# Optimization experiments

Hardware: AMD Instinct MI355X
Metric: run time of the kernel (lower is better)

Reference implementation:

```python
import jax, jax.numpy as jnp
import numpy as np

B, S, D = 2, 2048, 2048
H, DN, DR, DV, R = 16, 128, 64, 128, 512
EPS = 1e-6


def rmsnorm(x, g, eps=EPS):
    var = jnp.mean(x * x, axis=-1, keepdims=True)
    return x * jax.lax.rsqrt(var + eps) * g


def apply_rope(x, freqs):
    # x: [B,S,H,DR], freqs: [S, DR//2] angles. Complex-pair (interleaved) rotation.
    b, s, h, d = x.shape
    xp = x.reshape(b, s, h, d // 2, 2)
    xr, xi = xp[..., 0], xp[..., 1]
    cos = jnp.cos(freqs)[None, :, None, :]
    sin = jnp.sin(freqs)[None, :, None, :]
    outr = xr * cos - xi * sin
    outi = xr * sin + xi * cos
    return jnp.stack([outr, outi], axis=-1).reshape(b, s, h, d)


def setup_inputs() -> dict:
    key = jax.random.key(0)
    ks = jax.random.split(key, 8)
    x = jax.random.normal(ks[0], (B, S, D), dtype=jnp.float32)
    # RoPE angles: pos * inv_freq, standard theta=10000
    inv_freq = 1.0 / (10000.0 ** (np.arange(0, DR, 2, dtype=np.float32) / DR))
    freqs = jnp.asarray(np.arange(S, dtype=np.float32)[:, None] * inv_freq[None, :])
    sc = lambda fan_in: 1.0 / np.sqrt(fan_in)
    # weights stored [in, out] so forward is x @ W
    w_kv = jax.random.normal(ks[1], (D, R), dtype=jnp.float32) * sc(D)
    g_kv = jnp.ones((R,), dtype=jnp.float32)
    w_k = jax.random.normal(ks[2], (R, H * (DN + DR)), dtype=jnp.float32) * sc(R)
    w_v = jax.random.normal(ks[3], (R, H * DV), dtype=jnp.float32) * sc(R)
    w_qn = jax.random.normal(ks[4], (D, H * DN), dtype=jnp.float32) * sc(D)
    w_qr = jax.random.normal(ks[5], (D, H * DR), dtype=jnp.float32) * sc(D)
    w_o = jax.random.normal(ks[6], (H * DV, D), dtype=jnp.float32) * sc(H * DV)
    return {"x": x, "freqs": freqs, "w_kv": w_kv, "g_kv": g_kv, "w_k": w_k,
            "w_v": w_v, "w_qn": w_qn, "w_qr": w_qr, "w_o": w_o}


def reference(x, freqs, w_kv, g_kv, w_k, w_v, w_qn, w_qr, w_o):
    b, s, _ = x.shape
    # latent KV compression + RMSNorm
    kv = rmsnorm(x @ w_kv, g_kv)                       # [B,S,R]
    k_full = (kv @ w_k).reshape(b, s, H, DN + DR)      # [B,S,H,192]
    k_nope, k_rope = k_full[..., :DN], k_full[..., DN:]
    v = (kv @ w_v).reshape(b, s, H, DV)                # [B,S,H,DV]
    q_nope = (x @ w_qn).reshape(b, s, H, DN)
    q_rope = (x @ w_qr).reshape(b, s, H, DR)
    q_rope = apply_rope(q_rope, freqs)
    k_rope = apply_rope(k_rope, freqs)
    q = jnp.concatenate([q_nope, q_rope], axis=-1)     # [B,S,H,192]
    k = jnp.concatenate([k_nope, k_rope], axis=-1)
    scale = 1.0 / np.sqrt(DN + DR)
    scores = jnp.einsum('bshd,bthd->bhst', q, k) * scale  # [B,H,S,S]
    causal = jnp.tril(jnp.ones((s, s), dtype=bool))
    scores = jnp.where(causal[None, None], scores, jnp.float32(-1e30))
    attn = jax.nn.softmax(scores, axis=-1)
    out = jnp.einsum('bhst,bthd->bshd', attn, v).reshape(b, s, H * DV)
    return out @ w_o                                   # [B,S,D]
```

## Files before the change

### kernel.cpp

```cpp
#include <hip/hip_runtime.h>

typedef __bf16 bf16_t;
typedef bf16_t bf16x8 __attribute__((ext_vector_type(8)));
typedef bf16_t bf16x4v __attribute__((ext_vector_type(4)));
typedef float f32x4 __attribute__((ext_vector_type(4)));

#define GLDS16(g, l) __builtin_amdgcn_global_load_lds( \
    (const __attribute__((address_space(1))) void*)(g), \
    (__attribute__((address_space(3))) void*)(l), 16, 0, 0)

#define BB 2
#define SEQ 2048
#define DMODEL 2048
#define RDIM 512
#define NH 16
#define DNOPE 128
#define DROPE 64
#define DVDIM 128
#define MROWS 4096
#define DQK 192


__global__ __launch_bounds__(256) void cast_x_kernel(const float* __restrict__ x,
                                                     bf16_t* __restrict__ xb) {
    int idx = blockIdx.x * 256 + threadIdx.x;
    float4 v = ((const float4*)x)[idx];
    bf16x4v o;
    o[0] = (bf16_t)v.x; o[1] = (bf16_t)v.y; o[2] = (bf16_t)v.z; o[3] = (bf16_t)v.w;
    ((bf16x4v*)xb)[idx] = o;
}

__global__ __launch_bounds__(256) void wtrans_kernel(const float* __restrict__ W,
                                                     bf16_t* __restrict__ WT,
                                                     int K, int N) {
    __shared__ float t[32][33];
    int n0 = blockIdx.x * 32, k0 = blockIdx.y * 32;
    int tx = threadIdx.x & 31, ty = threadIdx.x >> 5;
    #pragma unroll
    for (int i = 0; i < 4; ++i)
        t[ty + i*8][tx] = W[(size_t)(k0 + ty + i*8) * N + n0 + tx];
    __syncthreads();
    #pragma unroll
    for (int i = 0; i < 4; ++i)
        WT[(size_t)(n0 + ty + i*8) * K + k0 + tx] = (bf16_t)t[tx][ty + i*8];
}

__global__ __launch_bounds__(256) void rope_table_kernel(const float* __restrict__ freqs,
                                                         float* __restrict__ costab,
                                                         float* __restrict__ sintab) {
    int idx = blockIdx.x * 256 + threadIdx.x;
    float f = freqs[idx];
    costab[idx] = cosf(f);
    sintab[idx] = sinf(f);
}

__global__ __launch_bounds__(256) void rmsnorm_kernel(const float* __restrict__ kvf,
                                                      const float* __restrict__ gkv,
                                                      bf16_t* __restrict__ kvb) {
    int m = blockIdx.x;
    int tid = threadIdx.x;
    const float* rowp = kvf + (size_t)m * RDIM;
    float2 v = *(const float2*)(rowp + tid * 2);
    float ss = v.x * v.x + v.y * v.y;
    #pragma unroll
    for (int d = 1; d < 64; d <<= 1) ss += __shfl_xor(ss, d, 64);
    __shared__ float red[4];
    if ((tid & 63) == 0) red[tid >> 6] = ss;
    __syncthreads();
    float tot = red[0] + red[1] + red[2] + red[3];
    float scale = rsqrtf(tot * (1.0f / RDIM) + 1e-6f);
    bf16_t* orow = kvb + (size_t)m * RDIM;
    orow[tid*2]     = (bf16_t)(v.x * scale * gkv[tid*2]);
    orow[tid*2 + 1] = (bf16_t)(v.y * scale * gkv[tid*2 + 1]);
}


template<typename OutT, int EPI>
__global__ __launch_bounds__(256, 2) void gemm_bt(const bf16_t* __restrict__ A,
                                                  const bf16_t* __restrict__ Bt,
                                                  OutT* __restrict__ C,
                                                  int M, int N, int K,
                                                  const float* __restrict__ costab,
                                                  const float* __restrict__ sintab) {
    __shared__ __align__(16) char ldsA[128 * 128];
    __shared__ __align__(16) char ldsB[128 * 128];
    int tid = threadIdx.x;
    int lane = tid & 63, wave = tid >> 6;
    int n0 = blockIdx.x * 128, m0 = blockIdx.y * 128;
    int wr = wave >> 1, wc = wave & 1;
    int g = lane >> 4, c = lane & 15;
    f32x4 acc[4][4] = {};

    int srow = tid >> 3;
    int sch = tid & 7;

    int nkt = K >> 6;
    for (int kt = 0; kt < nkt; ++kt) {
        int k0 = kt << 6;
        #pragma unroll
        for (int j = 0; j < 4; ++j) {
            int row = j * 32 + srow;
            int csrc = sch ^ (row & 7);
            const char* gA = (const char*)(A + (size_t)(m0 + row) * K + k0) + csrc * 16;
            const char* gB = (const char*)(Bt + (size_t)(n0 + row) * K + k0) + csrc * 16;
            char* lA = ldsA + j * 4096 + wave * 1024;
            char* lB = ldsB + j * 4096 + wave * 1024;
            GLDS16(gA, lA);
            GLDS16(gB, lB);
        }
        __syncthreads();
        #pragma unroll
        for (int kk = 0; kk < 2; ++kk) {
            int kb = kk * 64 + g * 16;
            bf16x8 aF[4], bF[4];
            #pragma unroll
            for (int m = 0; m < 4; ++m) {
                int row = wr * 64 + m * 16 + c;
                aF[m] = *(const bf16x8*)(ldsA + row * 128 + (kb ^ ((row & 7) << 4)));
            }
            #pragma unroll
            for (int n = 0; n < 4; ++n) {
                int row = wc * 64 + n * 16 + c;
                bF[n] = *(const bf16x8*)(ldsB + row * 128 + (kb ^ ((row & 7) << 4)));
            }
            #pragma unroll
            for (int m = 0; m < 4; ++m)
                #pragma unroll
                for (int n = 0; n < 4; ++n)
                    acc[m][n] = __builtin_amdgcn_mfma_f32_16x16x32_bf16(aF[m], bF[n], acc[m][n], 0, 0, 0);
        }
        __syncthreads();
    }
    #pragma unroll
    for (int m = 0; m < 4; ++m) {
        int grow0 = m0 + wr * 64 + m * 16 + g * 4;
        #pragma unroll
        for (int n = 0; n < 4; ++n) {
            int gcol = n0 + wc * 64 + n * 16 + c;
            bool rope = false;
            int j = 0;
            if (EPI == 1) {
                rope = (gcol < 3072) && ((gcol % 192) >= 128);
                j = ((gcol % 192) - 128) >> 1;
            } else if (EPI == 2) {
                rope = (gcol >= 2048);
                j = ((gcol - 2048) & 63) >> 1;
            }
            if (EPI != 0 && rope) {
                bool even = (c & 1) == 0;
                #pragma unroll
                for (int i = 0; i < 4; ++i) {
                    float v = acc[m][n][i];
                    float pv = __shfl_xor(v, 1, 64);
                    int s = (grow0 + i) & (SEQ - 1);
                    float cs = costab[s * 32 + j], sn = sintab[s * 32 + j];
                    float o = even ? (v * cs - pv * sn) : (pv * sn + v * cs);
                    C[(size_t)(grow0 + i) * N + gcol] = (OutT)o;
                }
            } else {
                #pragma unroll
                for (int i = 0; i < 4; ++i)
                    C[(size_t)(grow0 + i) * N + gcol] = (OutT)acc[m][n][i];
            }
        }
    }
}

__global__ __launch_bounds__(256) void pack_v_kernel(const bf16_t* __restrict__ kvout,
                                                     bf16_t* __restrict__ vt) {
    __shared__ bf16_t t[64][144];
    int blk = blockIdx.x;
    int bh = blk >> 5, st = blk & 31;
    int s0 = st * 64;
    int b = bh >> 4, h = bh & 15;
    int tid = threadIdx.x;
    #pragma unroll
    for (int i = 0; i < 4; ++i) {
        int id = i * 256 + tid;
        int row = id >> 4, ch = id & 15;
        bf16x8 v = *(const bf16x8*)(kvout + (size_t)(b * SEQ + s0 + row) * 5120 + 3072 + h * 128 + ch * 8);
        *(bf16x8*)&t[row][ch * 8] = v;
    }
    __syncthreads();
    #pragma unroll
    for (int i = 0; i < 4; ++i) {
        int id = i * 256 + tid;
        int dv = id >> 3, sc = id & 7;
        bf16x8 v;
        #pragma unroll
        for (int jj = 0; jj < 8; ++jj) v[jj] = t[sc * 8 + jj][dv];
        *(bf16x8*)(vt + ((size_t)bh * 128 + dv) * SEQ + s0 + sc * 8) = v;
    }
}


__global__ __launch_bounds__(512, 2) void attn_kernel(const bf16_t* __restrict__ Qf,
                                                      const bf16_t* __restrict__ KV,
                                                      const bf16_t* __restrict__ VT,
                                                      bf16_t* __restrict__ O) {
    __shared__ __align__(16) char ldsK[2 * 64 * 384];
    __shared__ __align__(16) char ldsV[2 * 128 * 128];
    __shared__ __align__(16) char ldsP[8 * 16 * 176];
    int tid = threadIdx.x, lane = tid & 63, wave = tid >> 6;
    int g = lane >> 4, c = lane & 15;

    int bid = blockIdx.x;
    int xcd = bid & 7, r = bid >> 3;
    int bh = xcd * 4 + (r & 3);
    int p = r >> 2;
    int b = bh >> 4, h = bh & 15;

    const bf16_t* Kb = KV + (size_t)b * SEQ * 5120 + h * DQK;
    const bf16_t* Vb = VT + (size_t)bh * 128 * SEQ;
    char* ldsPw = ldsP + wave * (16 * 176);

    size_t soff[3];
    #pragma unroll
    for (int i2 = 0; i2 < 3; ++i2) {
        int id = i2 * 512 + tid;
        int row = id / 24, ch = id - row * 24;
        soff[i2] = (size_t)row * 10240 + (ch ^ (row & 7)) * 16;
    }
    size_t voff[2];
    #pragma unroll
    for (int i2 = 0; i2 < 2; ++i2) {
        int id = i2 * 512 + tid;
        int row = id >> 3, ch = id & 7;
        voff[i2] = (size_t)row * (SEQ * 2) + (ch ^ (row & 7)) * 16;
    }
    const float sc = 0.0721687836f * 1.44269504f;

    bf16x8 vones;
    #pragma unroll
    for (int j = 0; j < 8; ++j) vones[j] = (bf16_t)1.0f;

    #pragma unroll 1
    for (int pass = 0; pass < 2; ++pass) {
        int qt = pass ? p : (15 - p);
        int q0 = qt * 128;
        int nt = 2 * qt + 2;
        int tdiag = 2 * qt + (wave >> 2);

        bf16x8 qf[6];
        {
            int qrow = q0 + wave * 16 + c;
            const bf16_t* qn = Qf + (size_t)(b * SEQ + qrow) * 3072 + h * DNOPE + g * 8;
            #pragma unroll
            for (int kk = 0; kk < 4; ++kk) qf[kk] = *(const bf16x8*)(qn + kk * 32);
            const bf16_t* qr = Qf + (size_t)(b * SEQ + qrow) * 3072 + 2048 + h * DROPE + g * 8;
            qf[4] = *(const bf16x8*)(qr);
            qf[5] = *(const bf16x8*)(qr + 32);
        }
        float m_run[4];
        f32x4 accO[9] = {};
        #pragma unroll
        for (int i = 0; i < 4; ++i) m_run[i] = -3.0e38f;

        {
            const char* Kt = (const char*)(Kb);
            #pragma unroll
            for (int i2 = 0; i2 < 3; ++i2)
                GLDS16(Kt + soff[i2], ldsK + i2 * 8192 + wave * 1024);
            const char* Vt = (const char*)Vb;
            #pragma unroll
            for (int i2 = 0; i2 < 2; ++i2)
                GLDS16(Vt + voff[i2], ldsV + i2 * 8192 + wave * 1024);
        }
        __syncthreads();

        #pragma unroll 1
        for (int t = 0; t < nt; ++t) {
            int cur = t & 1;
            if (t + 1 < nt) {
                int nxt = cur ^ 1;
                const char* Kt = (const char*)(Kb + (size_t)(t + 1) * 64 * 5120);
                #pragma unroll
                for (int i2 = 0; i2 < 3; ++i2)
                    GLDS16(Kt + soff[i2], ldsK + nxt * 24576 + i2 * 8192 + wave * 1024);
                const char* Vt = (const char*)Vb + (size_t)(t + 1) * 128;
                #pragma unroll
                for (int i2 = 0; i2 < 2; ++i2)
                    GLDS16(Vt + voff[i2], ldsV + nxt * 16384 + i2 * 8192 + wave * 1024);
            }

            if (t <= tdiag) {
                bool diag = (t == tdiag);
                const char* ldsKc = ldsK + cur * 24576;
                const char* ldsVc = ldsV + cur * 16384;

                f32x4 accS[4] = {};
                __builtin_amdgcn_s_setprio(1);
                #pragma unroll
                for (int kk = 0; kk < 6; ++kk) {
                    int kb = kk * 64 + g * 16;
                    #pragma unroll
                    for (int n = 0; n < 4; ++n) {
                        int row = n * 16 + c;
                        bf16x8 kf = *(const bf16x8*)(ldsKc + row * 384 + (kb ^ ((row & 7) << 4)));
                        accS[n] = __builtin_amdgcn_mfma_f32_16x16x32_bf16(qf[kk], kf, accS[n], 0, 0, 0);
                    }
                }
                __builtin_amdgcn_s_setprio(0);

                #pragma unroll
                for (int n = 0; n < 4; ++n)
                    #pragma unroll
                    for (int i = 0; i < 4; ++i) {
                        float v = accS[n][i] * sc;
                        if (diag && (n * 16 + c > (wave & 3) * 16 + g * 4 + i)) v = -1e30f;
                        accS[n][i] = v;
                    }
                float mx[4];
                #pragma unroll
                for (int i = 0; i < 4; ++i) {
                    float m2 = fmaxf(fmaxf(accS[0][i], accS[1][i]), fmaxf(accS[2][i], accS[3][i]));
                    #pragma unroll
                    for (int d = 1; d < 16; d <<= 1) m2 = fmaxf(m2, __shfl_xor(m2, d, 64));
                    mx[i] = m2;
                }
                bool nore = __all((mx[0] <= m_run[0] + 8.f) & (mx[1] <= m_run[1] + 8.f) &
                                  (mx[2] <= m_run[2] + 8.f) & (mx[3] <= m_run[3] + 8.f));
                if (nore) {
                    #pragma unroll
                    for (int i = 0; i < 4; ++i)
                        #pragma unroll
                        for (int n = 0; n < 4; ++n)
                            accS[n][i] = exp2f(accS[n][i] - m_run[i]);
                } else {
                    #pragma unroll
                    for (int i = 0; i < 4; ++i) {
                        float mnew = fmaxf(m_run[i], mx[i]);
                        float alpha = exp2f(m_run[i] - mnew);
                        m_run[i] = mnew;
                        #pragma unroll
                        for (int n = 0; n < 4; ++n)
                            accS[n][i] = exp2f(accS[n][i] - mnew);
                        #pragma unroll
                        for (int n = 0; n < 9; ++n) accO[n][i] *= alpha;
                    }
                }
                #pragma unroll
                for (int n = 0; n < 4; ++n)
                    #pragma unroll
                    for (int i = 0; i < 4; ++i)
                        *(bf16_t*)(ldsPw + (g * 4 + i) * 176 + (n * 16 + c) * 2) = (bf16_t)accS[n][i];
                bf16x8 pf0 = *(const bf16x8*)(ldsPw + c * 176 + g * 16);
                bf16x8 pf1 = *(const bf16x8*)(ldsPw + c * 176 + 64 + g * 16);

                __builtin_amdgcn_s_setprio(1);
                #pragma unroll
                for (int n = 0; n < 8; ++n) {
                    int row = n * 16 + c;
                    bf16x8 vf0 = *(const bf16x8*)(ldsVc + row * 128 + ((g * 16) ^ ((c & 7) << 4)));
                    bf16x8 vf1 = *(const bf16x8*)(ldsVc + row * 128 + ((64 + g * 16) ^ ((c & 7) << 4)));
                    accO[n] = __builtin_amdgcn_mfma_f32_16x16x32_bf16(pf0, vf0, accO[n], 0, 0, 0);
                    accO[n] = __builtin_amdgcn_mfma_f32_16x16x32_bf16(pf1, vf1, accO[n], 0, 0, 0);
                }
                accO[8] = __builtin_amdgcn_mfma_f32_16x16x32_bf16(pf0, vones, accO[8], 0, 0, 0);
                accO[8] = __builtin_amdgcn_mfma_f32_16x16x32_bf16(pf1, vones, accO[8], 0, 0, 0);
                __builtin_amdgcn_s_setprio(0);
            }
            __syncthreads();
        }
        float inv_l[4];
        #pragma unroll
        for (int i = 0; i < 4; ++i) inv_l[i] = 1.0f / accO[8][i];
        #pragma unroll
        for (int n = 0; n < 8; ++n) {
            int gcol = h * 128 + n * 16 + c;
            #pragma unroll
            for (int i = 0; i < 4; ++i) {
                int mrow = b * SEQ + q0 + wave * 16 + g * 4 + i;
                O[(size_t)mrow * 2048 + gcol] = (bf16_t)(accO[n][i] * inv_l[i]);
            }
        }
        __syncthreads();
    }
}


extern "C" void kernel_launch(void* const* d_in, const int* in_sizes, int n_in,
                              void* d_out, int out_size, void* d_ws, size_t ws_size,
                              hipStream_t stream) {
    const float* x     = (const float*)d_in[0];
    const float* freqs = (const float*)d_in[1];
    const float* w_kv  = (const float*)d_in[2];
    const float* g_kv  = (const float*)d_in[3];
    const float* w_k   = (const float*)d_in[4];
    const float* w_v   = (const float*)d_in[5];
    const float* w_qn  = (const float*)d_in[6];
    const float* w_qr  = (const float*)d_in[7];
    const float* w_o   = (const float*)d_in[8];
    float* out = (float*)d_out;

    char* ws = (char*)d_ws;
    size_t off = 0;
    auto alloc = [&](size_t bytes) { char* p = ws + off; off += (bytes + 255) & ~(size_t)255; return p; };
    bf16_t* xb     = (bf16_t*)alloc((size_t)MROWS * DMODEL * 2);
    bf16_t* wkvT   = (bf16_t*)alloc((size_t)RDIM * DMODEL * 2);
    bf16_t* wkvwT  = (bf16_t*)alloc((size_t)5120 * RDIM * 2);
    bf16_t* wqT    = (bf16_t*)alloc((size_t)3072 * DMODEL * 2);
    bf16_t* woT    = (bf16_t*)alloc((size_t)DMODEL * DMODEL * 2);
    float*  kvf    = (float*) alloc((size_t)MROWS * RDIM * 4);
    bf16_t* kvb    = (bf16_t*)alloc((size_t)MROWS * RDIM * 2);
    bf16_t* kvout  = (bf16_t*)alloc((size_t)MROWS * 5120 * 2);
    bf16_t* qfull  = (bf16_t*)alloc((size_t)MROWS * 3072 * 2);
    bf16_t* vt     = (bf16_t*)alloc((size_t)32 * 128 * SEQ * 2);
    bf16_t* attno  = (bf16_t*)alloc((size_t)MROWS * 2048 * 2);
    float*  costab = (float*) alloc((size_t)SEQ * 32 * 4);
    float*  sintab = (float*) alloc((size_t)SEQ * 32 * 4);

    cast_x_kernel<<<(MROWS * DMODEL / 4) / 256, 256, 0, stream>>>(x, xb);
    wtrans_kernel<<<dim3(RDIM / 32, DMODEL / 32), 256, 0, stream>>>(w_kv, wkvT, DMODEL, RDIM);
    wtrans_kernel<<<dim3(3072 / 32, RDIM / 32), 256, 0, stream>>>(w_k, wkvwT, RDIM, 3072);
    wtrans_kernel<<<dim3(2048 / 32, RDIM / 32), 256, 0, stream>>>(w_v, wkvwT + (size_t)3072 * RDIM, RDIM, 2048);
    wtrans_kernel<<<dim3(2048 / 32, DMODEL / 32), 256, 0, stream>>>(w_qn, wqT, DMODEL, 2048);
    wtrans_kernel<<<dim3(1024 / 32, DMODEL / 32), 256, 0, stream>>>(w_qr, wqT + (size_t)2048 * DMODEL, DMODEL, 1024);
    wtrans_kernel<<<dim3(2048 / 32, DMODEL / 32), 256, 0, stream>>>(w_o, woT, DMODEL, 2048);
    rope_table_kernel<<<(SEQ * 32) / 256, 256, 0, stream>>>(freqs, costab, sintab);

    gemm_bt<float, 0><<<dim3(RDIM / 128, MROWS / 128), 256, 0, stream>>>(xb, wkvT, kvf, MROWS, RDIM, DMODEL, nullptr, nullptr);
    rmsnorm_kernel<<<MROWS, 256, 0, stream>>>(kvf, g_kv, kvb);
    gemm_bt<bf16_t, 1><<<dim3(5120 / 128, MROWS / 128), 256, 0, stream>>>(kvb, wkvwT, kvout, MROWS, 5120, RDIM, costab, sintab);
    gemm_bt<bf16_t, 2><<<dim3(3072 / 128, MROWS / 128), 256, 0, stream>>>(xb, wqT, qfull, MROWS, 3072, DMODEL, costab, sintab);

    pack_v_kernel<<<32 * 32, 256, 0, stream>>>(kvout, vt);

    attn_kernel<<<256, 512, 0, stream>>>(qfull, kvout, vt, attno);

    gemm_bt<float, 0><<<dim3(2048 / 128, MROWS / 128), 256, 0, stream>>>(attno, woT, out, MROWS, 2048, DMODEL, nullptr, nullptr);
}
```

Measured before the change: 324.2 us.

## Fuse KV-down and Q projections into one GEMM; triple-buffer attention K/V loads

Concatenates w_kv, w_qn and w_qr into one transposed weight so a single GEMM over x produces both the latent KV (fp32) and rope'd Q (bf16) through a new split epilogue. This removes a second full pass over x and a launch, and avoids the under-filled 512-column GEMM grid. The attention kernel moves from double to triple buffering of K/V tiles, using explicit vmcnt waits and one barrier per iteration in place of a trailing __syncthreads. It also pre-scales Q by the softmax scale so the per-element scale multiply is dropped. The extra LDS lowers the headroom for occupancy, and rounding Q after scaling slightly changes numerics.

After: 304.4 us. 6.1% less time.

```diff
diff --git a/kernel.cpp b/kernel.cpp
--- a/kernel.cpp
+++ b/kernel.cpp
@@ -81,7 +81,8 @@
                                                   OutT* __restrict__ C,
                                                   int M, int N, int K,
                                                   const float* __restrict__ costab,
-                                                  const float* __restrict__ sintab) {
+                                                  const float* __restrict__ sintab,
+                                                  bf16_t* __restrict__ C2) {
     __shared__ __align__(16) char ldsA[128 * 128];
     __shared__ __align__(16) char ldsB[128 * 128];
     int tid = threadIdx.x;
@@ -137,30 +138,57 @@
         #pragma unroll
         for (int n = 0; n < 4; ++n) {
             int gcol = n0 + wc * 64 + n * 16 + c;
-            bool rope = false;
-            int j = 0;
-            if (EPI == 1) {
-                rope = (gcol < 3072) && ((gcol % 192) >= 128);
-                j = ((gcol % 192) - 128) >> 1;
-            } else if (EPI == 2) {
-                rope = (gcol >= 2048);
-                j = ((gcol - 2048) & 63) >> 1;
-            }
-            if (EPI != 0 && rope) {
-                bool even = (c & 1) == 0;
-                #pragma unroll
-                for (int i = 0; i < 4; ++i) {
-                    float v = acc[m][n][i];
-                    float pv = __shfl_xor(v, 1, 64);
-                    int s = (grow0 + i) & (SEQ - 1);
-                    float cs = costab[s * 32 + j], sn = sintab[s * 32 + j];
-                    float o = even ? (v * cs - pv * sn) : (pv * sn + v * cs);
-                    C[(size_t)(grow0 + i) * N + gcol] = (OutT)o;
+            if (EPI == 3) {
+                if (gcol < 512) {
+                    #pragma unroll
+                    for (int i = 0; i < 4; ++i)
+                        C[(size_t)(grow0 + i) * 512 + gcol] = (OutT)acc[m][n][i];
+                } else {
+                    int qcol = gcol - 512;
+                    if (qcol >= 2048) {
+                        int j = ((qcol - 2048) & 63) >> 1;
+                        bool even = (c & 1) == 0;
+                        #pragma unroll
+                        for (int i = 0; i < 4; ++i) {
+                            float v = acc[m][n][i];
+                            float pv = __shfl_xor(v, 1, 64);
+                            int s = (grow0 + i) & (SEQ - 1);
+                            float cs = costab[s * 32 + j], sn = sintab[s * 32 + j];
+                            float o = even ? (v * cs - pv * sn) : (pv * sn + v * cs);
+                            C2[(size_t)(grow0 + i) * 3072 + qcol] = (bf16_t)o;
+                        }
+                    } else {
+                        #pragma unroll
+                        for (int i = 0; i < 4; ++i)
+                            C2[(size_t)(grow0 + i) * 3072 + qcol] = (bf16_t)acc[m][n][i];
+                    }
                 }
             } else {
-                #pragma unroll
-                for (int i = 0; i < 4; ++i)
-                    C[(size_t)(grow0 + i) * N + gcol] = (OutT)acc[m][n][i];
+                bool rope = false;
+                int j = 0;
+                if (EPI == 1) {
+                    rope = (gcol < 3072) && ((gcol % 192) >= 128);
+                    j = ((gcol % 192) - 128) >> 1;
+                } else if (EPI == 2) {
+                    rope = (gcol >= 2048);
+                    j = ((gcol - 2048) & 63) >> 1;
+                }
+                if (EPI != 0 && rope) {
+                    bool even = (c & 1) == 0;
+                    #pragma unroll
+                    for (int i = 0; i < 4; ++i) {
+                        float v = acc[m][n][i];
+                        float pv = __shfl_xor(v, 1, 64);
+                        int s = (grow0 + i) & (SEQ - 1);
+                        float cs = costab[s * 32 + j], sn = sintab[s * 32 + j];
+                        float o = even ? (v * cs - pv * sn) : (pv * sn + v * cs);
+                        C[(size_t)(grow0 + i) * N + gcol] = (OutT)o;
+                    }
+                } else {
+                    #pragma unroll
+                    for (int i = 0; i < 4; ++i)
+                        C[(size_t)(grow0 + i) * N + gcol] = (OutT)acc[m][n][i];
+                }
             }
         }
     }
@@ -198,8 +226,8 @@
                                                       const bf16_t* __restrict__ KV,
                                                       const bf16_t* __restrict__ VT,
                                                       bf16_t* __restrict__ O) {
-    __shared__ __align__(16) char ldsK[2 * 64 * 384];
-    __shared__ __align__(16) char ldsV[2 * 128 * 128];
+    __shared__ __align__(16) char ldsK[3 * 64 * 384];
+    __shared__ __align__(16) char ldsV[3 * 128 * 128];
     __shared__ __align__(16) char ldsP[8 * 16 * 176];
     int tid = threadIdx.x, lane = tid & 63, wave = tid >> 6;
     int g = lane >> 4, c = lane & 15;
@@ -233,6 +261,17 @@
     bf16x8 vones;
     #pragma unroll
     for (int j = 0; j < 8; ++j) vones[j] = (bf16_t)1.0f;
+
+    auto stage = [&](int t, int buf) {
+        const char* Kt = (const char*)(Kb + (size_t)t * 64 * 5120);
+        #pragma unroll
+        for (int i2 = 0; i2 < 3; ++i2)
+            GLDS16(Kt + soff[i2], ldsK + buf * 24576 + i2 * 8192 + wave * 1024);
+        const char* Vt = (const char*)Vb + (size_t)t * 128;
+        #pragma unroll
+        for (int i2 = 0; i2 < 2; ++i2)
+            GLDS16(Vt + voff[i2], ldsV + buf * 16384 + i2 * 8192 + wave * 1024);
+    };
 
     #pragma unroll 1
     for (int pass = 0; pass < 2; ++pass) {
@@ -250,38 +289,29 @@
             const bf16_t* qr = Qf + (size_t)(b * SEQ + qrow) * 3072 + 2048 + h * DROPE + g * 8;
             qf[4] = *(const bf16x8*)(qr);
             qf[5] = *(const bf16x8*)(qr + 32);
+            #pragma unroll
+            for (int kk = 0; kk < 6; ++kk)
+                #pragma unroll
+                for (int j = 0; j < 8; ++j)
+                    qf[kk][j] = (bf16_t)((float)qf[kk][j] * sc);
         }
         float m_run[4];
         f32x4 accO[9] = {};
         #pragma unroll
         for (int i = 0; i < 4; ++i) m_run[i] = -3.0e38f;
 
-        {
-            const char* Kt = (const char*)(Kb);
-            #pragma unroll
-            for (int i2 = 0; i2 < 3; ++i2)
-                GLDS16(Kt + soff[i2], ldsK + i2 * 8192 + wave * 1024);
-            const char* Vt = (const char*)Vb;
-            #pragma unroll
-            for (int i2 = 0; i2 < 2; ++i2)
-                GLDS16(Vt + voff[i2], ldsV + i2 * 8192 + wave * 1024);
-        }
-        __syncthreads();
+        stage(0, 0);
+        stage(1, 1);
 
         #pragma unroll 1
         for (int t = 0; t < nt; ++t) {
-            int cur = t & 1;
-            if (t + 1 < nt) {
-                int nxt = cur ^ 1;
-                const char* Kt = (const char*)(Kb + (size_t)(t + 1) * 64 * 5120);
-                #pragma unroll
-                for (int i2 = 0; i2 < 3; ++i2)
-                    GLDS16(Kt + soff[i2], ldsK + nxt * 24576 + i2 * 8192 + wave * 1024);
-                const char* Vt = (const char*)Vb + (size_t)(t + 1) * 128;
-                #pragma unroll
-                for (int i2 = 0; i2 < 2; ++i2)
-                    GLDS16(Vt + voff[i2], ldsV + nxt * 16384 + i2 * 8192 + wave * 1024);
-            }
+            int cur = t - (t / 3) * 3;
+            if (t + 1 < nt) asm volatile("s_waitcnt vmcnt(5)" ::: "memory");
+            else            asm volatile("s_waitcnt vmcnt(0)" ::: "memory");
+            __builtin_amdgcn_s_barrier();
+            __builtin_amdgcn_sched_barrier(0);
+            asm volatile("" ::: "memory");
+            if (t + 2 < nt) stage(t + 2, (t + 2) % 3);
 
             if (t <= tdiag) {
                 bool diag = (t == tdiag);
@@ -302,14 +332,13 @@
                 }
                 __builtin_amdgcn_s_setprio(0);
 
-                #pragma unroll
-                for (int n = 0; n < 4; ++n)
-                    #pragma unroll
-                    for (int i = 0; i < 4; ++i) {
-                        float v = accS[n][i] * sc;
-                        if (diag && (n * 16 + c > (wave & 3) * 16 + g * 4 + i)) v = -1e30f;
-                        accS[n][i] = v;
-                    }
+                if (diag) {
+                    #pragma unroll
+                    for (int n = 0; n < 4; ++n)
+                        #pragma unroll
+                        for (int i = 0; i < 4; ++i)
+                            if (n * 16 + c > (wave & 3) * 16 + g * 4 + i) accS[n][i] = -1e30f;
+                }
                 float mx[4];
                 #pragma unroll
                 for (int i = 0; i < 4; ++i) {
@@ -360,7 +389,6 @@
                 accO[8] = __builtin_amdgcn_mfma_f32_16x16x32_bf16(pf1, vones, accO[8], 0, 0, 0);
                 __builtin_amdgcn_s_setprio(0);
             }
-            __syncthreads();
         }
         float inv_l[4];
         #pragma unroll
@@ -397,9 +425,8 @@
     size_t off = 0;
     auto alloc = [&](size_t bytes) { char* p = ws + off; off += (bytes + 255) & ~(size_t)255; return p; };
     bf16_t* xb     = (bf16_t*)alloc((size_t)MROWS * DMODEL * 2);
-    bf16_t* wkvT   = (bf16_t*)alloc((size_t)RDIM * DMODEL * 2);
+    bf16_t* wqkT   = (bf16_t*)alloc((size_t)3584 * DMODEL * 2);
     bf16_t* wkvwT  = (bf16_t*)alloc((size_t)5120 * RDIM * 2);
-    bf16_t* wqT    = (bf16_t*)alloc((size_t)3072 * DMODEL * 2);
     bf16_t* woT    = (bf16_t*)alloc((size_t)DMODEL * DMODEL * 2);
     float*  kvf    = (float*) alloc((size_t)MROWS * RDIM * 4);
     bf16_t* kvb    = (bf16_t*)alloc((size_t)MROWS * RDIM * 2);
@@ -411,22 +438,24 @@
     float*  sintab = (float*) alloc((size_t)SEQ * 32 * 4);
 
     cast_x_kernel<<<(MROWS * DMODEL / 4) / 256, 256, 0, stream>>>(x, xb);
-    wtrans_kernel<<<dim3(RDIM / 32, DMODEL / 32), 256, 0, stream>>>(w_kv, wkvT, DMODEL, RDIM);
+    wtrans_kernel<<<dim3(RDIM / 32, DMODEL / 32), 256, 0, stream>>>(w_kv, wqkT, DMODEL, RDIM);
+    wtrans_kernel<<<dim3(2048 / 32, DMODEL / 32), 256, 0, stream>>>(w_qn, wqkT + (size_t)512 * DMODEL, DMODEL, 2048);
+    wtrans_kernel<<<dim3(1024 / 32, DMODEL / 32), 256, 0, stream>>>(w_qr, wqkT + (size_t)2560 * DMODEL, DMODEL, 1024);
     wtrans_kernel<<<dim3(3072 / 32, RDIM / 32), 256, 0, stream>>>(w_k, wkvwT, RDIM, 3072);
     wtrans_kernel<<<dim3(2048 / 32, RDIM / 32), 256, 0, stream>>>(w_v, wkvwT + (size_t)3072 * RDIM, RDIM, 2048);
-    wtrans_kernel<<<dim3(2048 / 32, DMODEL / 32), 256, 0, stream>>>(w_qn, wqT, DMODEL, 2048);
-    wtrans_kernel<<<dim3(1024 / 32, DMODEL / 32), 256, 0, stream>>>(w_qr, wqT + (size_t)2048 * DMODEL, DMODEL, 1024);
     wtrans_kernel<<<dim3(2048 / 32, DMODEL / 32), 256, 0, stream>>>(w_o, woT, DMODEL, 2048);
     rope_table_kernel<<<(SEQ * 32) / 256, 256, 0, stream>>>(freqs, costab, sintab);
 
-    gemm_bt<float, 0><<<dim3(RDIM / 128, MROWS / 128), 256, 0, stream>>>(xb, wkvT, kvf, MROWS, RDIM, DMODEL, nullptr, nullptr);
+    gemm_bt<float, 3><<<dim3(3584 / 128, MROWS / 128), 256, 0, stream>>>(
+        xb, wqkT, kvf, MROWS, 3584, DMODEL, costab, sintab, qfull);
     rmsnorm_kernel<<<MROWS, 256, 0, stream>>>(kvf, g_kv, kvb);
-    gemm_bt<bf16_t, 1><<<dim3(5120 / 128, MROWS / 128), 256, 0, stream>>>(kvb, wkvwT, kvout, MROWS, 5120, RDIM, costab, sintab);
-    gemm_bt<bf16_t, 2><<<dim3(3072 / 128, MROWS / 128), 256, 0, stream>>>(xb, wqT, qfull, MROWS, 3072, DMODEL, costab, sintab);
+    gemm_bt<bf16_t, 1><<<dim3(5120 / 128, MROWS / 128), 256, 0, stream>>>(
+        kvb, wkvwT, kvout, MROWS, 5120, RDIM, costab, sintab, nullptr);
 
     pack_v_kernel<<<32 * 32, 256, 0, stream>>>(kvout, vt);
 
     attn_kernel<<<256, 512, 0, stream>>>(qfull, kvout, vt, attno);
 
-    gemm_bt<float, 0><<<dim3(2048 / 128, MROWS / 128), 256, 0, stream>>>(attno, woT, out, MROWS, 2048, DMODEL, nullptr, nullptr);
-}
+    gemm_bt<float, 0><<<dim3(2048 / 128, MROWS / 128), 256, 0, stream>>>(
+        attno, woT, out, MROWS, 2048, DMODEL, nullptr, nullptr, nullptr);
+}
```
